# Kernel tuning notes

Measured on AMD Instinct MI355X. Metric: run time of the kernel, lower is better.

The kernel has to match this reference:

```python
import jax, jax.numpy as jnp
import numpy as np

N_NODES = 50000
N_EDGES = 800000
D = 128          # embedding_dim
G = 3            # group_size
K = 4            # window_size
ALPHA = -0.5
WEIGHTS = (1.0, 1.0, 7.81, 45.28)
EPS = 1e-12      # torch F.normalize clamp_min


def _striped_projection(key):
    """Striped sparse random projection, densified (matches torch coalesce+to_dense)."""
    num_groups = D // G  # 42; columns 126..127 remain zero, as in the original
    k_off, k_sign = jax.random.split(key)
    row_idx = jnp.repeat(jnp.arange(N_NODES), num_groups)
    base = jnp.tile(jnp.arange(0, num_groups * G, G), N_NODES)
    off = jax.random.randint(k_off, (N_NODES * num_groups,), 0, G)
    col_idx = base + off
    scale = float(np.sqrt(G))  # 1/sqrt(density), density = 1/g
    vals = (jax.random.randint(k_sign, (N_NODES * num_groups,), 0, 2).astype(jnp.float32) * 2.0 - 1.0) * scale
    return jnp.zeros((N_NODES, D), jnp.float32).at[row_idx, col_idx].add(vals)


def setup_inputs() -> dict:
    key = jax.random.key(0)
    k1, k2, k3 = jax.random.split(key, 3)
    edge_row = jax.random.randint(k1, (N_EDGES,), 0, N_NODES)
    edge_col = jax.random.randint(k2, (N_EDGES,), 0, N_NODES)
    edge_val = jnp.ones((N_EDGES,), jnp.float32)
    R = _striped_projection(k3)
    return {"edge_row": edge_row, "edge_col": edge_col, "edge_val": edge_val, "R": R}


def reference(edge_row, edge_col, edge_val, R):
    N = R.shape[0]
    # degrees = row sums of sparse adjacency; zeros -> 1
    deg = jax.ops.segment_sum(edge_val, edge_row, num_segments=N)
    deg = jnp.where(deg == 0, 1.0, deg)
    # initial degree scaling: N_curr = R * deg**alpha
    x = R * (deg ** ALPHA)[:, None]
    inv_deg = (1.0 / deg)[:, None]
    acc = jnp.zeros_like(R)
    for i in range(K):
        # SpMM: out[r] = sum_{e: row[e]==r} val[e] * x[col[e]]
        x = jax.ops.segment_sum(edge_val[:, None] * x[edge_col], edge_row, num_segments=N)
        x = x * inv_deg  # transition-matrix ('trans') scaling
        nrm = jnp.maximum(jnp.sqrt(jnp.sum(x * x, axis=1, keepdims=True)), EPS)
        acc = acc + (x / nrm) * WEIGHTS[i]
    mean = acc.mean(axis=0)
    std = jnp.std(acc, axis=0, ddof=1)  # torch .std() is unbiased
    std = jnp.where(std == 0, 1.0, std)
    return (acc - mean) / std
```

## Files before the change

### kernel.cpp

```cpp
#include <hip/hip_runtime.h>
#include <math.h>

#define NN 50000
#define NE 800000
#define DD 128
#define NBKT 196
#define BCAP 5120
#define CHUNK 2048
#define NCHUNK ((NE + CHUNK - 1) / CHUNK)
#define SPMM_NBLK (NN / 16)

static __device__ __forceinline__ float blo(unsigned int p) { return __uint_as_float(p << 16); }
static __device__ __forceinline__ float bhi(unsigned int p) { return __uint_as_float(p & 0xffff0000u); }
static __device__ __forceinline__ unsigned int pack2bf(float a, float b) {
    unsigned int ua = __float_as_uint(a);
    unsigned int ub = __float_as_uint(b);
    ua = ua + 0x7FFFu + ((ua >> 16) & 1u);
    ub = ub + 0x7FFFu + ((ub >> 16) & 1u);
    return (ua >> 16) | (ub & 0xffff0000u);
}

static __global__ __launch_bounds__(256) void bin_kernel(
    const int* __restrict__ erow, const int* __restrict__ ecol, const float* __restrict__ eval_,
    int* __restrict__ bucket_cursor, uint2* __restrict__ binned) {
    __shared__ uint2 sorted[CHUNK];
    __shared__ unsigned short sbin[CHUNK];
    __shared__ int hist[NBKT];
    __shared__ int bstart[NBKT];
    __shared__ int bcur[NBKT];
    __shared__ int gbase[NBKT];
    __shared__ int tmp[256];

    int t = threadIdx.x;
    int cbase = blockIdx.x * CHUNK;
    int cn = NE - cbase; if (cn > CHUNK) cn = CHUNK;

    for (int i = t; i < NBKT; i += 256) hist[i] = 0;
    __syncthreads();

    unsigned int rc[8]; unsigned int vv[8]; int bb[8];
    int nloc = 0;
    for (int i = t; i < cn; i += 256) {
        int g = cbase + i;
        int r = erow[g];
        int c = ecol[g];
        float v = eval_[g];
        rc[nloc] = (unsigned)r | ((unsigned)c << 16);
        vv[nloc] = __float_as_uint(v);
        int b = r >> 8;
        bb[nloc] = b;
        atomicAdd(&hist[b], 1);
        ++nloc;
    }
    __syncthreads();

    int hv = (t < NBKT) ? hist[t] : 0;
    tmp[t] = hv;
    __syncthreads();
    for (int off = 1; off < 256; off <<= 1) {
        int u = (t >= off) ? tmp[t - off] : 0;
        __syncthreads();
        tmp[t] += u;
        __syncthreads();
    }
    if (t < NBKT) {
        int ex = tmp[t] - hv;
        bstart[t] = ex;
        bcur[t] = ex;
        gbase[t] = atomicAdd(&bucket_cursor[t], hv);
    }
    __syncthreads();

    for (int k = 0; k < nloc; ++k) {
        int pos = atomicAdd(&bcur[bb[k]], 1);
        sorted[pos] = make_uint2(rc[k], vv[k]);
        sbin[pos] = (unsigned short)bb[k];
    }
    __syncthreads();

    for (int i = t; i < cn; i += 256) {
        int b = sbin[i];
        binned[(size_t)b * BCAP + gbase[b] + (i - bstart[b])] = sorted[i];
    }
}

static __global__ __launch_bounds__(256) void sort_kernel(
    const uint2* __restrict__ binned, const int* __restrict__ bucket_cursor,
    uint2* __restrict__ csr, int* __restrict__ row_start, float* __restrict__ deg,
    const float* __restrict__ R, uint4* __restrict__ x0) {
    __shared__ uint2 buf[BCAP];
    __shared__ int hist[256];
    __shared__ int rcur[256];
    __shared__ float fdeg[256];
    __shared__ int pscan[256];
    int b = blockIdx.x;
    int t = threadIdx.x;
    int lo = b << 8;

    int pv = (t < NBKT) ? bucket_cursor[t] : 0;
    pscan[t] = pv;
    hist[t] = 0;
    fdeg[t] = 0.0f;
    __syncthreads();
    for (int off = 1; off < 256; off <<= 1) {
        int u = (t >= off) ? pscan[t - off] : 0;
        __syncthreads();
        pscan[t] += u;
        __syncthreads();
    }
    int gb = (b == 0) ? 0 : pscan[b - 1];
    int cnt = pscan[b] - gb;

    for (int i = t; i < cnt; i += 256) {
        uint2 e = binned[(size_t)b * BCAP + i];
        buf[i] = e;
        int rr = (int)(e.x & 0xFFFFu) - lo;
        atomicAdd(&hist[rr], 1);
        atomicAdd(&fdeg[rr], __uint_as_float(e.y));
    }
    __syncthreads();
    int hv = hist[t];
    rcur[t] = hv;
    __syncthreads();
    for (int off = 1; off < 256; off <<= 1) {
        int u = (t >= off) ? rcur[t - off] : 0;
        __syncthreads();
        rcur[t] += u;
        __syncthreads();
    }
    int excl = rcur[t] - hv;
    int r = lo + t;
    if (r < NN) {
        row_start[r] = gb + excl;
        float d = fdeg[t];
        deg[r] = (d == 0.0f) ? 1.0f : d;
    }
    if (b == NBKT - 1 && t == 255) row_start[NN] = gb + cnt;
    rcur[t] = excl;
    __syncthreads();
    for (int i = t; i < cnt; i += 256) {
        uint2 e = buf[i];
        int rr = (int)(e.x & 0xFFFFu) - lo;
        int pos = atomicAdd(&rcur[rr], 1);
        csr[(size_t)gb + pos] = make_uint2(e.x >> 16, e.y);
    }

    int nrows = NN - lo; if (nrows > 256) nrows = 256;
    const float4* __restrict__ R4 = (const float4*)R;
    for (int idx = t; idx < nrows * 16; idx += 256) {
        int rr = idx >> 4;
        int sub = idx & 15;
        float d = fdeg[rr];
        d = (d == 0.0f) ? 1.0f : d;
        float sc = rsqrtf(d);
        size_t g = (size_t)(lo + rr) * 16 + sub;
        float4 f0 = R4[g * 2];
        float4 f1 = R4[g * 2 + 1];
        x0[g] = make_uint4(pack2bf(f0.x * sc, f0.y * sc), pack2bf(f0.z * sc, f0.w * sc),
                           pack2bf(f1.x * sc, f1.y * sc), pack2bf(f1.z * sc, f1.w * sc));
    }
}

static __global__ __launch_bounds__(256) void spmm_fused_kernel(
    const int* __restrict__ row_start, const uint2* __restrict__ csr,
    const uint4* __restrict__ x4, const float* __restrict__ deg,
    uint4* __restrict__ x_next4, float* __restrict__ s_out, float weight) {
    int wave = threadIdx.x >> 6;
    int lane = threadIdx.x & 63;
    int quarter = lane >> 4;
    int sub = lane & 15;
    int row = blockIdx.x * 16 + wave * 4 + quarter;
    int s = row_start[row];
    int e = row_start[row + 1];

    float a0 = 0.f, a1 = 0.f, a2 = 0.f, a3 = 0.f, a4 = 0.f, a5 = 0.f, a6 = 0.f, a7 = 0.f;
    for (int base = s; base < e; base += 16) {
        int j = base + sub;
        int cl = 0;
        float vl = 0.0f;
        if (j < e) { uint2 t2 = csr[j]; cl = (int)t2.x; vl = __uint_as_float(t2.y); }
        int cnt = e - base; if (cnt > 16) cnt = 16;
        for (int k = 0; k < cnt; k += 4) {
            int l0 = quarter * 16 + k;
            int c0 = __shfl(cl, l0);
            int c1 = __shfl(cl, l0 + 1);
            int c2 = __shfl(cl, l0 + 2);
            int c3 = __shfl(cl, l0 + 3);
            float v0 = __shfl(vl, l0);
            float v1 = __shfl(vl, l0 + 1);
            float v2 = __shfl(vl, l0 + 2);
            float v3 = __shfl(vl, l0 + 3);
            uint4 p0 = x4[(size_t)c0 * 16 + sub];
            uint4 p1 = x4[(size_t)c1 * 16 + sub];
            uint4 p2 = x4[(size_t)c2 * 16 + sub];
            uint4 p3 = x4[(size_t)c3 * 16 + sub];
            a0 += v0 * blo(p0.x); a1 += v0 * bhi(p0.x); a2 += v0 * blo(p0.y); a3 += v0 * bhi(p0.y);
            a4 += v0 * blo(p0.z); a5 += v0 * bhi(p0.z); a6 += v0 * blo(p0.w); a7 += v0 * bhi(p0.w);
            a0 += v1 * blo(p1.x); a1 += v1 * bhi(p1.x); a2 += v1 * blo(p1.y); a3 += v1 * bhi(p1.y);
            a4 += v1 * blo(p1.z); a5 += v1 * bhi(p1.z); a6 += v1 * blo(p1.w); a7 += v1 * bhi(p1.w);
            a0 += v2 * blo(p2.x); a1 += v2 * bhi(p2.x); a2 += v2 * blo(p2.y); a3 += v2 * bhi(p2.y);
            a4 += v2 * blo(p2.z); a5 += v2 * bhi(p2.z); a6 += v2 * blo(p2.w); a7 += v2 * bhi(p2.w);
            a0 += v3 * blo(p3.x); a1 += v3 * bhi(p3.x); a2 += v3 * blo(p3.y); a3 += v3 * bhi(p3.y);
            a4 += v3 * blo(p3.z); a5 += v3 * bhi(p3.z); a6 += v3 * blo(p3.w); a7 += v3 * bhi(p3.w);
        }
    }

    float id = 1.0f / deg[row];
    a0 *= id; a1 *= id; a2 *= id; a3 *= id; a4 *= id; a5 *= id; a6 *= id; a7 *= id;

    float ss = a0 * a0 + a1 * a1 + a2 * a2 + a3 * a3 + a4 * a4 + a5 * a5 + a6 * a6 + a7 * a7;
#pragma unroll
    for (int m = 1; m <= 8; m <<= 1) ss += __shfl_xor(ss, m);
    float nrm = fmaxf(sqrtf(ss), 1e-12f);

    x_next4[(size_t)row * 16 + sub] = make_uint4(pack2bf(a0, a1), pack2bf(a2, a3),
                                                 pack2bf(a4, a5), pack2bf(a6, a7));
    if (sub == 0) s_out[row] = weight / nrm;
}

static __global__ __launch_bounds__(256) void spmm_last_kernel(
    const int* __restrict__ row_start, const uint2* __restrict__ csr,
    const uint4* __restrict__ xin, const float* __restrict__ deg,
    const uint4* __restrict__ x1, const uint4* __restrict__ x2, const uint4* __restrict__ x3,
    const float* __restrict__ s1, const float* __restrict__ s2, const float* __restrict__ s3,
    float* __restrict__ out, float* __restrict__ psum, float* __restrict__ psumsq, float weight) {
    __shared__ float shs[256 * 8];
    __shared__ float shq[256 * 8];
    int wave = threadIdx.x >> 6;
    int lane = threadIdx.x & 63;
    int quarter = lane >> 4;
    int sub = lane & 15;
    int row = blockIdx.x * 16 + wave * 4 + quarter;
    int s = row_start[row];
    int e = row_start[row + 1];

    float a0 = 0.f, a1 = 0.f, a2 = 0.f, a3 = 0.f, a4 = 0.f, a5 = 0.f, a6 = 0.f, a7 = 0.f;
    for (int base = s; base < e; base += 16) {
        int j = base + sub;
        int cl = 0;
        float vl = 0.0f;
        if (j < e) { uint2 t2 = csr[j]; cl = (int)t2.x; vl = __uint_as_float(t2.y); }
        int cnt = e - base; if (cnt > 16) cnt = 16;
        for (int k = 0; k < cnt; k += 4) {
            int l0 = quarter * 16 + k;
            int c0 = __shfl(cl, l0);
            int c1 = __shfl(cl, l0 + 1);
            int c2 = __shfl(cl, l0 + 2);
            int c3 = __shfl(cl, l0 + 3);
            float v0 = __shfl(vl, l0);
            float v1 = __shfl(vl, l0 + 1);
            float v2 = __shfl(vl, l0 + 2);
            float v3 = __shfl(vl, l0 + 3);
            uint4 p0 = xin[(size_t)c0 * 16 + sub];
            uint4 p1 = xin[(size_t)c1 * 16 + sub];
            uint4 p2 = xin[(size_t)c2 * 16 + sub];
            uint4 p3 = xin[(size_t)c3 * 16 + sub];
            a0 += v0 * blo(p0.x); a1 += v0 * bhi(p0.x); a2 += v0 * blo(p0.y); a3 += v0 * bhi(p0.y);
            a4 += v0 * blo(p0.z); a5 += v0 * bhi(p0.z); a6 += v0 * blo(p0.w); a7 += v0 * bhi(p0.w);
            a0 += v1 * blo(p1.x); a1 += v1 * bhi(p1.x); a2 += v1 * blo(p1.y); a3 += v1 * bhi(p1.y);
            a4 += v1 * blo(p1.z); a5 += v1 * bhi(p1.z); a6 += v1 * blo(p1.w); a7 += v1 * bhi(p1.w);
            a0 += v2 * blo(p2.x); a1 += v2 * bhi(p2.x); a2 += v2 * blo(p2.y); a3 += v2 * bhi(p2.y);
            a4 += v2 * blo(p2.z); a5 += v2 * bhi(p2.z); a6 += v2 * blo(p2.w); a7 += v2 * bhi(p2.w);
            a0 += v3 * blo(p3.x); a1 += v3 * bhi(p3.x); a2 += v3 * blo(p3.y); a3 += v3 * bhi(p3.y);
            a4 += v3 * blo(p3.z); a5 += v3 * bhi(p3.z); a6 += v3 * blo(p3.w); a7 += v3 * bhi(p3.w);
        }
    }

    float id = 1.0f / deg[row];
    a0 *= id; a1 *= id; a2 *= id; a3 *= id; a4 *= id; a5 *= id; a6 *= id; a7 *= id;

    float ss = a0 * a0 + a1 * a1 + a2 * a2 + a3 * a3 + a4 * a4 + a5 * a5 + a6 * a6 + a7 * a7;
#pragma unroll
    for (int m = 1; m <= 8; m <<= 1) ss += __shfl_xor(ss, m);
    float nrm = fmaxf(sqrtf(ss), 1e-12f);
    float w4 = weight / nrm;

    size_t xi = (size_t)row * 16 + sub;
    float w1 = s1[row], w2 = s2[row], w3 = s3[row];
    uint4 q1 = x1[xi], q2 = x2[xi], q3 = x3[xi];
    float v[8];
    v[0] = w1 * blo(q1.x) + w2 * blo(q2.x) + w3 * blo(q3.x) + w4 * a0;
    v[1] = w1 * bhi(q1.x) + w2 * bhi(q2.x) + w3 * bhi(q3.x) + w4 * a1;
    v[2] = w1 * blo(q1.y) + w2 * blo(q2.y) + w3 * blo(q3.y) + w4 * a2;
    v[3] = w1 * bhi(q1.y) + w2 * bhi(q2.y) + w3 * bhi(q3.y) + w4 * a3;
    v[4] = w1 * blo(q1.z) + w2 * blo(q2.z) + w3 * blo(q3.z) + w4 * a4;
    v[5] = w1 * bhi(q1.z) + w2 * bhi(q2.z) + w3 * bhi(q3.z) + w4 * a5;
    v[6] = w1 * blo(q1.w) + w2 * blo(q2.w) + w3 * blo(q3.w) + w4 * a6;
    v[7] = w1 * bhi(q1.w) + w2 * bhi(q2.w) + w3 * bhi(q3.w) + w4 * a7;

    float4* out4 = (float4*)out;
    out4[(size_t)row * 32 + sub * 2]     = make_float4(v[0], v[1], v[2], v[3]);
    out4[(size_t)row * 32 + sub * 2 + 1] = make_float4(v[4], v[5], v[6], v[7]);

    int t = threadIdx.x;
#pragma unroll
    for (int j = 0; j < 8; ++j) {
        shs[t * 8 + j] = v[j];
        shq[t * 8 + j] = v[j] * v[j];
    }
    __syncthreads();
    if (t < DD) {
        int cs = t >> 3, cj = t & 7;
        float sacc = 0.0f, qacc = 0.0f;
        for (int g = 0; g < 16; ++g) {
            int src = (g * 16 + cs) * 8 + cj;
            sacc += shs[src];
            qacc += shq[src];
        }
        psum[(size_t)blockIdx.x * DD + t] = sacc;
        psumsq[(size_t)blockIdx.x * DD + t] = qacc;
    }
}

static __global__ __launch_bounds__(256) void fold_kernel(
    const float* __restrict__ psum, const float* __restrict__ psumsq,
    float* __restrict__ mean, float* __restrict__ invstd) {
    __shared__ double ss[256], qq[256];
    int c = blockIdx.x;
    int t = threadIdx.x;
    double s = 0.0, q = 0.0;
    for (int b = t; b < SPMM_NBLK; b += 256) {
        s += (double)psum[(size_t)b * DD + c];
        q += (double)psumsq[(size_t)b * DD + c];
    }
    ss[t] = s; qq[t] = q;
    __syncthreads();
    for (int off = 128; off > 0; off >>= 1) {
        if (t < off) { ss[t] += ss[t + off]; qq[t] += qq[t + off]; }
        __syncthreads();
    }
    if (t == 0) {
        double m = ss[0] / (double)NN;
        double var = (qq[0] - (double)NN * m * m) / (double)(NN - 1);
        if (var < 0.0) var = 0.0;
        double sd = sqrt(var);
        if (sd == 0.0) sd = 1.0;
        mean[c] = (float)m;
        invstd[c] = (float)(1.0 / sd);
    }
}

static __global__ __launch_bounds__(256) void normalize_kernel(
    float* __restrict__ out, const float* __restrict__ mean, const float* __restrict__ invstd) {
    int i = blockIdx.x * blockDim.x + threadIdx.x;
    int c4 = i & 31;
    float4 m = ((const float4*)mean)[c4];
    float4 is = ((const float4*)invstd)[c4];
    float4* out4 = (float4*)out;
    float4 v = out4[i];
    v.x = (v.x - m.x) * is.x;
    v.y = (v.y - m.y) * is.y;
    v.z = (v.z - m.z) * is.z;
    v.w = (v.w - m.w) * is.w;
    out4[i] = v;
}

extern "C" void kernel_launch(void* const* d_in, const int* in_sizes, int n_in,
                              void* d_out, int out_size, void* d_ws, size_t ws_size,
                              hipStream_t stream) {
    const int* erow = (const int*)d_in[0];
    const int* ecol = (const int*)d_in[1];
    const float* eval_ = (const float*)d_in[2];
    const float* R = (const float*)d_in[3];
    float* out = (float*)d_out;

    char* ws = (char*)d_ws;
    size_t off = 0;
    auto alloc = [&](size_t bytes) -> char* {
        char* p = ws + off;
        off += (bytes + 255) & ~(size_t)255;
        return p;
    };
    float* deg          = (float*)alloc(NN * sizeof(float));
    int* bucket_cursor  = (int*)alloc(NBKT * sizeof(int));
    int* row_start      = (int*)alloc((NN + 1) * sizeof(int));
    uint2* binned       = (uint2*)alloc((size_t)NBKT * BCAP * sizeof(uint2));
    uint2* csr          = (uint2*)alloc((size_t)NE * sizeof(uint2));
    uint4* x0           = (uint4*)alloc((size_t)NN * 16 * sizeof(uint4));
    uint4* x1           = (uint4*)alloc((size_t)NN * 16 * sizeof(uint4));
    uint4* x2           = (uint4*)alloc((size_t)NN * 16 * sizeof(uint4));
    uint4* x3           = (uint4*)alloc((size_t)NN * 16 * sizeof(uint4));
    float* s1           = (float*)alloc(NN * sizeof(float));
    float* s2           = (float*)alloc(NN * sizeof(float));
    float* s3           = (float*)alloc(NN * sizeof(float));
    float* psum         = (float*)alloc((size_t)SPMM_NBLK * DD * sizeof(float));
    float* psumsq       = (float*)alloc((size_t)SPMM_NBLK * DD * sizeof(float));
    float* meanbuf      = (float*)alloc(DD * sizeof(float));
    float* invstdb      = (float*)alloc(DD * sizeof(float));

    hipMemsetAsync(bucket_cursor, 0, NBKT * sizeof(int), stream);

    bin_kernel<<<NCHUNK, 256, 0, stream>>>(erow, ecol, eval_, bucket_cursor, binned);
    sort_kernel<<<NBKT, 256, 0, stream>>>(binned, bucket_cursor, csr, row_start, deg, R, x0);

    spmm_fused_kernel<<<SPMM_NBLK, 256, 0, stream>>>(row_start, csr, x0, deg, x1, s1, 1.0f);
    spmm_fused_kernel<<<SPMM_NBLK, 256, 0, stream>>>(row_start, csr, x1, deg, x2, s2, 1.0f);
    spmm_fused_kernel<<<SPMM_NBLK, 256, 0, stream>>>(row_start, csr, x2, deg, x3, s3, 7.81f);
    spmm_last_kernel<<<SPMM_NBLK, 256, 0, stream>>>(row_start, csr, x3, deg, x1, x2, x3,
                                                    s1, s2, s3, out, psum, psumsq, 45.28f);

    fold_kernel<<<DD, 256, 0, stream>>>(psum, psumsq, meanbuf, invstdb);
    normalize_kernel<<<NN * 32 / 256, 256, 0, stream>>>(out, meanbuf, invstdb);
}
```

Before: 256.1 us.

## Split SpMM feature columns into four quarter-planes for cache-friendly gathers

```diff
diff --git a/kernel.cpp b/kernel.cpp
--- a/kernel.cpp
+++ b/kernel.cpp
@@ -9,6 +9,12 @@
 #define CHUNK 2048
 #define NCHUNK ((NE + CHUNK - 1) / CHUNK)
 #define SPMM_NBLK (NN / 16)
+#define NQBLK (8 * ((SPMM_NBLK + 1) / 2))
+
+#define W1 1.0f
+#define W2 1.0f
+#define W3 7.81f
+#define W4 45.28f
 
 static __device__ __forceinline__ float blo(unsigned int p) { return __uint_as_float(p << 16); }
 static __device__ __forceinline__ float bhi(unsigned int p) { return __uint_as_float(p & 0xffff0000u); }
@@ -149,36 +155,45 @@
     const float4* __restrict__ R4 = (const float4*)R;
     for (int idx = t; idx < nrows * 16; idx += 256) {
         int rr = idx >> 4;
-        int sub = idx & 15;
+        int s = idx & 15;
         float d = fdeg[rr];
         d = (d == 0.0f) ? 1.0f : d;
         float sc = rsqrtf(d);
-        size_t g = (size_t)(lo + rr) * 16 + sub;
+        int node = lo + rr;
+        size_t g = (size_t)node * 16 + s;
         float4 f0 = R4[g * 2];
         float4 f1 = R4[g * 2 + 1];
-        x0[g] = make_uint4(pack2bf(f0.x * sc, f0.y * sc), pack2bf(f0.z * sc, f0.w * sc),
-                           pack2bf(f1.x * sc, f1.y * sc), pack2bf(f1.z * sc, f1.w * sc));
-    }
-}
-
-static __global__ __launch_bounds__(256) void spmm_fused_kernel(
+        size_t gq = ((size_t)(s >> 2) * NN + (size_t)node) * 4 + (size_t)(s & 3);
+        x0[gq] = make_uint4(pack2bf(f0.x * sc, f0.y * sc), pack2bf(f0.z * sc, f0.w * sc),
+                            pack2bf(f1.x * sc, f1.y * sc), pack2bf(f1.z * sc, f1.w * sc));
+    }
+}
+
+static __global__ __launch_bounds__(256) void spmm_q_kernel(
     const int* __restrict__ row_start, const uint2* __restrict__ csr,
-    const uint4* __restrict__ x4, const float* __restrict__ deg,
-    uint4* __restrict__ x_next4, float* __restrict__ s_out, float weight) {
+    const unsigned int* __restrict__ xq, const float* __restrict__ deg,
+    unsigned int* __restrict__ xout, unsigned int* __restrict__ xfull,
+    float* __restrict__ ssbuf) {
+    int b = blockIdx.x;
+    int q = (b & 7) >> 1;
+    int rblk = ((b >> 3) << 1) + (b & 1);
+    if (rblk >= SPMM_NBLK) return;
     int wave = threadIdx.x >> 6;
     int lane = threadIdx.x & 63;
     int quarter = lane >> 4;
     int sub = lane & 15;
-    int row = blockIdx.x * 16 + wave * 4 + quarter;
+    int row = rblk * 16 + wave * 4 + quarter;
     int s = row_start[row];
     int e = row_start[row + 1];
-
-    float a0 = 0.f, a1 = 0.f, a2 = 0.f, a3 = 0.f, a4 = 0.f, a5 = 0.f, a6 = 0.f, a7 = 0.f;
+    size_t qbase = (size_t)q * NN * 16;
+
+    float a0 = 0.f, a1 = 0.f;
     for (int base = s; base < e; base += 16) {
         int j = base + sub;
-        int cl = 0;
-        float vl = 0.0f;
-        if (j < e) { uint2 t2 = csr[j]; cl = (int)t2.x; vl = __uint_as_float(t2.y); }
+        unsigned long long pkt = 0ull;
+        if (j < e) pkt = __builtin_nontemporal_load((const unsigned long long*)csr + j);
+        int cl = (int)(unsigned int)pkt;
+        float vl = __uint_as_float((unsigned int)(pkt >> 32));
         int cnt = e - base; if (cnt > 16) cnt = 16;
         for (int k = 0; k < cnt; k += 4) {
             int l0 = quarter * 16 + k;
@@ -190,40 +205,40 @@
             float v1 = __shfl(vl, l0 + 1);
             float v2 = __shfl(vl, l0 + 2);
             float v3 = __shfl(vl, l0 + 3);
-            uint4 p0 = x4[(size_t)c0 * 16 + sub];
-            uint4 p1 = x4[(size_t)c1 * 16 + sub];
-            uint4 p2 = x4[(size_t)c2 * 16 + sub];
-            uint4 p3 = x4[(size_t)c3 * 16 + sub];
-            a0 += v0 * blo(p0.x); a1 += v0 * bhi(p0.x); a2 += v0 * blo(p0.y); a3 += v0 * bhi(p0.y);
-            a4 += v0 * blo(p0.z); a5 += v0 * bhi(p0.z); a6 += v0 * blo(p0.w); a7 += v0 * bhi(p0.w);
-            a0 += v1 * blo(p1.x); a1 += v1 * bhi(p1.x); a2 += v1 * blo(p1.y); a3 += v1 * bhi(p1.y);
-            a4 += v1 * blo(p1.z); a5 += v1 * bhi(p1.z); a6 += v1 * blo(p1.w); a7 += v1 * bhi(p1.w);
-            a0 += v2 * blo(p2.x); a1 += v2 * bhi(p2.x); a2 += v2 * blo(p2.y); a3 += v2 * bhi(p2.y);
-            a4 += v2 * blo(p2.z); a5 += v2 * bhi(p2.z); a6 += v2 * blo(p2.w); a7 += v2 * bhi(p2.w);
-            a0 += v3 * blo(p3.x); a1 += v3 * bhi(p3.x); a2 += v3 * blo(p3.y); a3 += v3 * bhi(p3.y);
-            a4 += v3 * blo(p3.z); a5 += v3 * bhi(p3.z); a6 += v3 * blo(p3.w); a7 += v3 * bhi(p3.w);
+            unsigned int u0 = xq[qbase + (size_t)c0 * 16 + sub];
+            unsigned int u1 = xq[qbase + (size_t)c1 * 16 + sub];
+            unsigned int u2 = xq[qbase + (size_t)c2 * 16 + sub];
+            unsigned int u3 = xq[qbase + (size_t)c3 * 16 + sub];
+            a0 += v0 * blo(u0); a1 += v0 * bhi(u0);
+            a0 += v1 * blo(u1); a1 += v1 * bhi(u1);
+            a0 += v2 * blo(u2); a1 += v2 * bhi(u2);
+            a0 += v3 * blo(u3); a1 += v3 * bhi(u3);
         }
     }
 
     float id = 1.0f / deg[row];
-    a0 *= id; a1 *= id; a2 *= id; a3 *= id; a4 *= id; a5 *= id; a6 *= id; a7 *= id;
-
-    float ss = a0 * a0 + a1 * a1 + a2 * a2 + a3 * a3 + a4 * a4 + a5 * a5 + a6 * a6 + a7 * a7;
+    a0 *= id; a1 *= id;
+
+    float ss = a0 * a0 + a1 * a1;
 #pragma unroll
     for (int m = 1; m <= 8; m <<= 1) ss += __shfl_xor(ss, m);
-    float nrm = fmaxf(sqrtf(ss), 1e-12f);
-
-    x_next4[(size_t)row * 16 + sub] = make_uint4(pack2bf(a0, a1), pack2bf(a2, a3),
-                                                 pack2bf(a4, a5), pack2bf(a6, a7));
-    if (sub == 0) s_out[row] = weight / nrm;
+
+    unsigned int pk = pack2bf(a0, a1);
+    if (xout) {
+        __builtin_nontemporal_store(pk, &xout[qbase + (size_t)row * 16 + sub]);
+    } else {
+        __builtin_nontemporal_store(pk, &xfull[(size_t)row * 64 + (size_t)(q * 16 + sub)]);
+    }
+    if (sub == 0) ssbuf[q * NN + row] = ss;
 }
 
 static __global__ __launch_bounds__(256) void spmm_last_kernel(
     const int* __restrict__ row_start, const uint2* __restrict__ csr,
     const uint4* __restrict__ xin, const float* __restrict__ deg,
-    const uint4* __restrict__ x1, const uint4* __restrict__ x2, const uint4* __restrict__ x3,
-    const float* __restrict__ s1, const float* __restrict__ s2, const float* __restrict__ s3,
-    float* __restrict__ out, float* __restrict__ psum, float* __restrict__ psumsq, float weight) {
+    const unsigned int* __restrict__ x1q, const unsigned int* __restrict__ x2q,
+    const uint4* __restrict__ x3f,
+    const float* __restrict__ ssb1, const float* __restrict__ ssb2, const float* __restrict__ ssb3,
+    float* __restrict__ out, float* __restrict__ psum, float* __restrict__ psumsq) {
     __shared__ float shs[256 * 8];
     __shared__ float shq[256 * 8];
     int wave = threadIdx.x >> 6;
@@ -237,9 +252,10 @@
     float a0 = 0.f, a1 = 0.f, a2 = 0.f, a3 = 0.f, a4 = 0.f, a5 = 0.f, a6 = 0.f, a7 = 0.f;
     for (int base = s; base < e; base += 16) {
         int j = base + sub;
-        int cl = 0;
-        float vl = 0.0f;
-        if (j < e) { uint2 t2 = csr[j]; cl = (int)t2.x; vl = __uint_as_float(t2.y); }
+        unsigned long long pkt = 0ull;
+        if (j < e) pkt = __builtin_nontemporal_load((const unsigned long long*)csr + j);
+        int cl = (int)(unsigned int)pkt;
+        float vl = __uint_as_float((unsigned int)(pkt >> 32));
         int cnt = e - base; if (cnt > 16) cnt = 16;
         for (int k = 0; k < cnt; k += 4) {
             int l0 = quarter * 16 + k;
@@ -273,11 +289,22 @@
 #pragma unroll
     for (int m = 1; m <= 8; m <<= 1) ss += __shfl_xor(ss, m);
     float nrm = fmaxf(sqrtf(ss), 1e-12f);
-    float w4 = weight / nrm;
-
-    size_t xi = (size_t)row * 16 + sub;
-    float w1 = s1[row], w2 = s2[row], w3 = s3[row];
-    uint4 q1 = x1[xi], q2 = x2[xi], q3 = x3[xi];
+    float w4 = W4 / nrm;
+
+    float ss1 = ssb1[row] + ssb1[NN + row] + ssb1[2 * NN + row] + ssb1[3 * NN + row];
+    float ss2 = ssb2[row] + ssb2[NN + row] + ssb2[2 * NN + row] + ssb2[3 * NN + row];
+    float ss3 = ssb3[row] + ssb3[NN + row] + ssb3[2 * NN + row] + ssb3[3 * NN + row];
+    float w1 = W1 / fmaxf(sqrtf(ss1), 1e-12f);
+    float w2 = W2 / fmaxf(sqrtf(ss2), 1e-12f);
+    float w3 = W3 / fmaxf(sqrtf(ss3), 1e-12f);
+
+    const uint4* x1q4 = (const uint4*)x1q;
+    const uint4* x2q4 = (const uint4*)x2q;
+    size_t qi = ((size_t)(sub >> 2) * NN + (size_t)row) * 4 + (size_t)(sub & 3);
+    uint4 q1 = x1q4[qi];
+    uint4 q2 = x2q4[qi];
+    uint4 q3 = x3f[(size_t)row * 16 + sub];
+
     float v[8];
     v[0] = w1 * blo(q1.x) + w2 * blo(q2.x) + w3 * blo(q3.x) + w4 * a0;
     v[1] = w1 * bhi(q1.x) + w2 * bhi(q2.x) + w3 * bhi(q3.x) + w4 * a1;
@@ -376,13 +403,13 @@
     int* row_start      = (int*)alloc((NN + 1) * sizeof(int));
     uint2* binned       = (uint2*)alloc((size_t)NBKT * BCAP * sizeof(uint2));
     uint2* csr          = (uint2*)alloc((size_t)NE * sizeof(uint2));
-    uint4* x0           = (uint4*)alloc((size_t)NN * 16 * sizeof(uint4));
-    uint4* x1           = (uint4*)alloc((size_t)NN * 16 * sizeof(uint4));
-    uint4* x2           = (uint4*)alloc((size_t)NN * 16 * sizeof(uint4));
-    uint4* x3           = (uint4*)alloc((size_t)NN * 16 * sizeof(uint4));
-    float* s1           = (float*)alloc(NN * sizeof(float));
-    float* s2           = (float*)alloc(NN * sizeof(float));
-    float* s3           = (float*)alloc(NN * sizeof(float));
+    unsigned int* x0    = (unsigned int*)alloc((size_t)NN * 64 * sizeof(unsigned int));
+    unsigned int* x1    = (unsigned int*)alloc((size_t)NN * 64 * sizeof(unsigned int));
+    unsigned int* x2    = (unsigned int*)alloc((size_t)NN * 64 * sizeof(unsigned int));
+    unsigned int* x3    = (unsigned int*)alloc((size_t)NN * 64 * sizeof(unsigned int));
+    float* ssb1         = (float*)alloc((size_t)4 * NN * sizeof(float));
+    float* ssb2         = (float*)alloc((size_t)4 * NN * sizeof(float));
+    float* ssb3         = (float*)alloc((size_t)4 * NN * sizeof(float));
     float* psum         = (float*)alloc((size_t)SPMM_NBLK * DD * sizeof(float));
     float* psumsq       = (float*)alloc((size_t)SPMM_NBLK * DD * sizeof(float));
     float* meanbuf      = (float*)alloc(DD * sizeof(float));
@@ -391,13 +418,16 @@
     hipMemsetAsync(bucket_cursor, 0, NBKT * sizeof(int), stream);
 
     bin_kernel<<<NCHUNK, 256, 0, stream>>>(erow, ecol, eval_, bucket_cursor, binned);
-    sort_kernel<<<NBKT, 256, 0, stream>>>(binned, bucket_cursor, csr, row_start, deg, R, x0);
-
-    spmm_fused_kernel<<<SPMM_NBLK, 256, 0, stream>>>(row_start, csr, x0, deg, x1, s1, 1.0f);
-    spmm_fused_kernel<<<SPMM_NBLK, 256, 0, stream>>>(row_start, csr, x1, deg, x2, s2, 1.0f);
-    spmm_fused_kernel<<<SPMM_NBLK, 256, 0, stream>>>(row_start, csr, x2, deg, x3, s3, 7.81f);
-    spmm_last_kernel<<<SPMM_NBLK, 256, 0, stream>>>(row_start, csr, x3, deg, x1, x2, x3,
-                                                    s1, s2, s3, out, psum, psumsq, 45.28f);
+    sort_kernel<<<NBKT, 256, 0, stream>>>(binned, bucket_cursor, csr, row_start, deg, R,
+                                          (uint4*)x0);
+
+    spmm_q_kernel<<<NQBLK, 256, 0, stream>>>(row_start, csr, x0, deg, x1, nullptr, ssb1);
+    spmm_q_kernel<<<NQBLK, 256, 0, stream>>>(row_start, csr, x1, deg, x2, nullptr, ssb2);
+    spmm_q_kernel<<<NQBLK, 256, 0, stream>>>(row_start, csr, x2, deg, nullptr, x3, ssb3);
+
+    spmm_last_kernel<<<SPMM_NBLK, 256, 0, stream>>>(row_start, csr, (const uint4*)x3, deg,
+                                                    x1, x2, (const uint4*)x3,
+                                                    ssb1, ssb2, ssb3, out, psum, psumsq);
 
     fold_kernel<<<DD, 256, 0, stream>>>(psum, psumsq, meanbuf, invstdb);
     normalize_kernel<<<NN * 32 / 256, 256, 0, stream>>>(out, meanbuf, invstdb);
```

Measured after the change: 309.5 us. 1.21x slower.

## Rebalance row bucketing across more blocks and split x0 scaling into own kernel

Applied to the files above, without the earlier changes.

```diff
diff --git a/kernel.cpp b/kernel.cpp
--- a/kernel.cpp
+++ b/kernel.cpp
@@ -4,8 +4,9 @@
 #define NN 50000
 #define NE 800000
 #define DD 128
-#define NBKT 196
-#define BCAP 5120
+#define NBKT 256
+#define RPB 196
+#define BCAP 3840
 #define CHUNK 2048
 #define NCHUNK ((NE + CHUNK - 1) / CHUNK)
 #define SPMM_NBLK (NN / 16)
@@ -20,34 +21,34 @@
     return (ua >> 16) | (ub & 0xffff0000u);
 }
 
-static __global__ __launch_bounds__(256) void bin_kernel(
+static __global__ __launch_bounds__(512) void bin_kernel(
     const int* __restrict__ erow, const int* __restrict__ ecol, const float* __restrict__ eval_,
     int* __restrict__ bucket_cursor, uint2* __restrict__ binned) {
     __shared__ uint2 sorted[CHUNK];
-    __shared__ unsigned short sbin[CHUNK];
+    __shared__ unsigned char sbin[CHUNK];
     __shared__ int hist[NBKT];
     __shared__ int bstart[NBKT];
     __shared__ int bcur[NBKT];
     __shared__ int gbase[NBKT];
-    __shared__ int tmp[256];
+    __shared__ int tmp[NBKT];
 
     int t = threadIdx.x;
     int cbase = blockIdx.x * CHUNK;
     int cn = NE - cbase; if (cn > CHUNK) cn = CHUNK;
 
-    for (int i = t; i < NBKT; i += 256) hist[i] = 0;
-    __syncthreads();
-
-    unsigned int rc[8]; unsigned int vv[8]; int bb[8];
+    for (int i = t; i < NBKT; i += 512) hist[i] = 0;
+    __syncthreads();
+
+    unsigned int rc[4]; unsigned int vv[4]; int bb[4];
     int nloc = 0;
-    for (int i = t; i < cn; i += 256) {
+    for (int i = t; i < cn; i += 512) {
         int g = cbase + i;
         int r = erow[g];
         int c = ecol[g];
         float v = eval_[g];
         rc[nloc] = (unsigned)r | ((unsigned)c << 16);
         vv[nloc] = __float_as_uint(v);
-        int b = r >> 8;
+        int b = r / RPB;
         bb[nloc] = b;
         atomicAdd(&hist[b], 1);
         ++nloc;
@@ -55,12 +56,12 @@
     __syncthreads();
 
     int hv = (t < NBKT) ? hist[t] : 0;
-    tmp[t] = hv;
-    __syncthreads();
-    for (int off = 1; off < 256; off <<= 1) {
-        int u = (t >= off) ? tmp[t - off] : 0;
-        __syncthreads();
-        tmp[t] += u;
+    if (t < NBKT) tmp[t] = hv;
+    __syncthreads();
+    for (int off = 1; off < NBKT; off <<= 1) {
+        int u = (t < NBKT && t >= off) ? tmp[t - off] : 0;
+        __syncthreads();
+        if (t < NBKT) tmp[t] += u;
         __syncthreads();
     }
     if (t < NBKT) {
@@ -74,44 +75,42 @@
     for (int k = 0; k < nloc; ++k) {
         int pos = atomicAdd(&bcur[bb[k]], 1);
         sorted[pos] = make_uint2(rc[k], vv[k]);
-        sbin[pos] = (unsigned short)bb[k];
-    }
-    __syncthreads();
-
-    for (int i = t; i < cn; i += 256) {
+        sbin[pos] = (unsigned char)bb[k];
+    }
+    __syncthreads();
+
+    for (int i = t; i < cn; i += 512) {
         int b = sbin[i];
         binned[(size_t)b * BCAP + gbase[b] + (i - bstart[b])] = sorted[i];
     }
 }
 
-static __global__ __launch_bounds__(256) void sort_kernel(
+static __global__ __launch_bounds__(512) void sort_kernel(
     const uint2* __restrict__ binned, const int* __restrict__ bucket_cursor,
-    uint2* __restrict__ csr, int* __restrict__ row_start, float* __restrict__ deg,
-    const float* __restrict__ R, uint4* __restrict__ x0) {
+    uint2* __restrict__ csr, int* __restrict__ row_start, float* __restrict__ deg) {
     __shared__ uint2 buf[BCAP];
-    __shared__ int hist[256];
-    __shared__ int rcur[256];
-    __shared__ float fdeg[256];
-    __shared__ int pscan[256];
+    __shared__ int hist[RPB];
+    __shared__ int rcur[RPB];
+    __shared__ float fdeg[RPB];
+    __shared__ int pscan[NBKT];
     int b = blockIdx.x;
     int t = threadIdx.x;
-    int lo = b << 8;
+    int lo = b * RPB;
 
     int pv = (t < NBKT) ? bucket_cursor[t] : 0;
-    pscan[t] = pv;
-    hist[t] = 0;
-    fdeg[t] = 0.0f;
-    __syncthreads();
-    for (int off = 1; off < 256; off <<= 1) {
-        int u = (t >= off) ? pscan[t - off] : 0;
-        __syncthreads();
-        pscan[t] += u;
+    if (t < NBKT) pscan[t] = pv;
+    if (t < RPB) { hist[t] = 0; fdeg[t] = 0.0f; }
+    __syncthreads();
+    for (int off = 1; off < NBKT; off <<= 1) {
+        int u = (t < NBKT && t >= off) ? pscan[t - off] : 0;
+        __syncthreads();
+        if (t < NBKT) pscan[t] += u;
         __syncthreads();
     }
     int gb = (b == 0) ? 0 : pscan[b - 1];
     int cnt = pscan[b] - gb;
 
-    for (int i = t; i < cnt; i += 256) {
+    for (int i = t; i < cnt; i += 512) {
         uint2 e = binned[(size_t)b * BCAP + i];
         buf[i] = e;
         int rr = (int)(e.x & 0xFFFFu) - lo;
@@ -119,46 +118,45 @@
         atomicAdd(&fdeg[rr], __uint_as_float(e.y));
     }
     __syncthreads();
-    int hv = hist[t];
-    rcur[t] = hv;
-    __syncthreads();
-    for (int off = 1; off < 256; off <<= 1) {
-        int u = (t >= off) ? rcur[t - off] : 0;
-        __syncthreads();
-        rcur[t] += u;
-        __syncthreads();
-    }
-    int excl = rcur[t] - hv;
-    int r = lo + t;
-    if (r < NN) {
-        row_start[r] = gb + excl;
-        float d = fdeg[t];
-        deg[r] = (d == 0.0f) ? 1.0f : d;
-    }
-    if (b == NBKT - 1 && t == 255) row_start[NN] = gb + cnt;
-    rcur[t] = excl;
-    __syncthreads();
-    for (int i = t; i < cnt; i += 256) {
+    int hv = (t < RPB) ? hist[t] : 0;
+    if (t < RPB) rcur[t] = hv;
+    __syncthreads();
+    for (int off = 1; off < RPB; off <<= 1) {
+        int u = (t < RPB && t >= off) ? rcur[t - off] : 0;
+        __syncthreads();
+        if (t < RPB) rcur[t] += u;
+        __syncthreads();
+    }
+    if (t < RPB) {
+        int excl = rcur[t] - hv;
+        int r = lo + t;
+        if (r < NN) {
+            row_start[r] = gb + excl;
+            float d = fdeg[t];
+            deg[r] = (d == 0.0f) ? 1.0f : d;
+        }
+        rcur[t] = excl;
+    }
+    if (b == NBKT - 1 && t == 0) row_start[NN] = gb + cnt;
+    __syncthreads();
+    for (int i = t; i < cnt; i += 512) {
         uint2 e = buf[i];
         int rr = (int)(e.x & 0xFFFFu) - lo;
         int pos = atomicAdd(&rcur[rr], 1);
         csr[(size_t)gb + pos] = make_uint2(e.x >> 16, e.y);
     }
-
-    int nrows = NN - lo; if (nrows > 256) nrows = 256;
+}
+
+static __global__ __launch_bounds__(256) void x0_kernel(
+    const float* __restrict__ R, const float* __restrict__ deg, uint4* __restrict__ x0) {
+    int idx = blockIdx.x * 256 + threadIdx.x;
+    int row = idx >> 4;
+    float sc = rsqrtf(deg[row]);
     const float4* __restrict__ R4 = (const float4*)R;
-    for (int idx = t; idx < nrows * 16; idx += 256) {
-        int rr = idx >> 4;
-        int sub = idx & 15;
-        float d = fdeg[rr];
-        d = (d == 0.0f) ? 1.0f : d;
-        float sc = rsqrtf(d);
-        size_t g = (size_t)(lo + rr) * 16 + sub;
-        float4 f0 = R4[g * 2];
-        float4 f1 = R4[g * 2 + 1];
-        x0[g] = make_uint4(pack2bf(f0.x * sc, f0.y * sc), pack2bf(f0.z * sc, f0.w * sc),
-                           pack2bf(f1.x * sc, f1.y * sc), pack2bf(f1.z * sc, f1.w * sc));
-    }
+    float4 f0 = R4[(size_t)idx * 2];
+    float4 f1 = R4[(size_t)idx * 2 + 1];
+    x0[idx] = make_uint4(pack2bf(f0.x * sc, f0.y * sc), pack2bf(f0.z * sc, f0.w * sc),
+                         pack2bf(f1.x * sc, f1.y * sc), pack2bf(f1.z * sc, f1.w * sc));
 }
 
 static __global__ __launch_bounds__(256) void spmm_fused_kernel(
@@ -390,8 +388,9 @@
 
     hipMemsetAsync(bucket_cursor, 0, NBKT * sizeof(int), stream);
 
-    bin_kernel<<<NCHUNK, 256, 0, stream>>>(erow, ecol, eval_, bucket_cursor, binned);
-    sort_kernel<<<NBKT, 256, 0, stream>>>(binned, bucket_cursor, csr, row_start, deg, R, x0);
+    bin_kernel<<<NCHUNK, 512, 0, stream>>>(erow, ecol, eval_, bucket_cursor, binned);
+    sort_kernel<<<NBKT, 512, 0, stream>>>(binned, bucket_cursor, csr, row_start, deg);
+    x0_kernel<<<SPMM_NBLK, 256, 0, stream>>>(R, deg, x0);
 
     spmm_fused_kernel<<<SPMM_NBLK, 256, 0, stream>>>(row_start, csr, x0, deg, x1, s1, 1.0f);
     spmm_fused_kernel<<<SPMM_NBLK, 256, 0, stream>>>(row_start, csr, x1, deg, x2, s2, 1.0f);
```

Result: faster. 247.6 us (-3.3%).
